# Kernel optimization log

Measured on AMD Instinct MI355X. Metric: run time of the kernel, lower is better.

## Reference

```python
import jax, jax.numpy as jnp
import numpy as np

N_HEAD = 16
D_HEAD = 64
D_MODEL = 1024
SCALE = 1.0 / float(D_HEAD) ** 0.5
LN_EPS = 1e-5


def _rel_shift(x):
    # x: [b, n, i, j] -> Transformer-XL relative shift
    b, n, i, j = x.shape
    x = jnp.pad(x, ((0, 0), (0, 0), (0, 0), (1, 0)))  # zero-pad front of last dim
    x = x.reshape(b, n, j + 1, i)[:, :, 1:, :]
    return x.reshape(b, n, i, j)


def _layer_norm(x, g, b):
    mu = jnp.mean(x, axis=-1, keepdims=True)
    var = jnp.mean(jnp.square(x - mu), axis=-1, keepdims=True)
    return g * (x - mu) / jnp.sqrt(var + LN_EPS) + b


def setup_inputs() -> dict:
    key = jax.random.key(0)
    ks = jax.random.split(key, 8)
    qlen, bsz = 1024, 4
    w = jax.random.normal(ks[0], (qlen, bsz, D_MODEL), jnp.float32)
    r = jax.random.normal(ks[1], (qlen, D_MODEL), jnp.float32)
    r_w_bias = 0.02 * jax.random.normal(ks[2], (N_HEAD, D_HEAD), jnp.float32)
    r_r_bias = 0.02 * jax.random.normal(ks[3], (N_HEAD, D_HEAD), jnp.float32)
    attn_mask = jnp.triu(jnp.ones((qlen, qlen), bool), 1)  # causal, True = masked
    qkv_w = 0.02 * jax.random.normal(ks[4], (D_MODEL, 3 * N_HEAD * D_HEAD), jnp.float32)
    qkv_b = jnp.zeros((3 * N_HEAD * D_HEAD,), jnp.float32)
    rk_w = 0.02 * jax.random.normal(ks[5], (D_MODEL, N_HEAD * D_HEAD), jnp.float32)
    rk_b = jnp.zeros((N_HEAD * D_HEAD,), jnp.float32)
    o_w = 0.02 * jax.random.normal(ks[6], (N_HEAD * D_HEAD, D_MODEL), jnp.float32)
    o_b = jnp.zeros((D_MODEL,), jnp.float32)
    ln_g = jnp.ones((D_MODEL,), jnp.float32)
    ln_b = jnp.zeros((D_MODEL,), jnp.float32)
    return {"w": w, "r": r, "r_w_bias": r_w_bias, "r_r_bias": r_r_bias,
            "qkv_w": qkv_w, "qkv_b": qkv_b, "rk_w": rk_w, "rk_b": rk_b,
            "o_w": o_w, "o_b": o_b, "ln_g": ln_g, "ln_b": ln_b,
            "attn_mask": attn_mask}


def reference(w, r, r_w_bias, r_r_bias, qkv_w, qkv_b, rk_w, rk_b, o_w, o_b, ln_g, ln_b, attn_mask):
    qlen, bsz, _ = w.shape
    # post-lnorm path (pre_lnorm=False)
    heads = w @ qkv_w + qkv_b                       # [q, b, 3*H*D]
    q, k, v = jnp.split(heads, 3, axis=-1)
    q = q.reshape(qlen, bsz, N_HEAD, D_HEAD)
    k = k.reshape(qlen, bsz, N_HEAD, D_HEAD)
    v = v.reshape(qlen, bsz, N_HEAD, D_HEAD)
    rk = (r @ rk_w + rk_b).reshape(-1, N_HEAD, D_HEAD)  # [rlen, H, D]
    AC = jnp.einsum('ibnd,jbnd->bnij', q + r_w_bias, k)
    BD = _rel_shift(jnp.einsum('ibnd,jnd->bnij', q + r_r_bias, rk))
    score = SCALE * (AC + BD)                       # [b, H, q, k]
    score = jnp.where(attn_mask[None, None, :, :], -jnp.inf, score)
    prob = jax.nn.softmax(score, axis=-1)
    vec = jnp.einsum('bnij,jbnd->ibnd', prob, v).reshape(qlen, bsz, N_HEAD * D_HEAD)
    attn_out = vec @ o_w + o_b
    return _layer_norm(w + attn_out, ln_g, ln_b)
```

## Files before the change

### kernel.cpp

```cpp
#include <hip/hip_runtime.h>
#include <math.h>

#define QL 1024
#define BSZ 4
#define NH 16
#define DH 64
#define DM 1024
#define SCALE_F 0.125f

typedef __attribute__((ext_vector_type(8))) short bf16x8;
typedef __attribute__((ext_vector_type(4))) float f32x4;

__device__ __forceinline__ unsigned short f2bf(float f) {
  union { float f; unsigned int u; } c; c.f = f;
  unsigned int u = c.u;
  u += 0x7FFFu + ((u >> 16) & 1u);
  return (unsigned short)(u >> 16);
}
__device__ __forceinline__ float bf2f(unsigned short u) {
  union { unsigned int i; float f; } c; c.i = ((unsigned int)u) << 16;
  return c.f;
}
__device__ __forceinline__ float2 bfp2f(const unsigned short* p) {
  unsigned int u = *(const unsigned int*)p;
  union { unsigned int u; float f; } lo, hi;
  lo.u = (u & 0xFFFFu) << 16;
  hi.u = u & 0xFFFF0000u;
  return make_float2(lo.f, hi.f);
}

__device__ __forceinline__ void ld_lds16(const unsigned short* g, unsigned short* l) {
  __builtin_amdgcn_global_load_lds(
      (const __attribute__((address_space(1))) unsigned int*)g,
      (__attribute__((address_space(3))) unsigned int*)l, 16, 0, 0);
}

__device__ __forceinline__ bf16x8 frag64(const unsigned short* lds, int n, int s) {
  return *(const bf16x8*)(lds + n * 64 + ((s ^ (n & 7)) * 8));
}

template <int CTRL>
__device__ __forceinline__ float dpp_mv(float x) {
  return __int_as_float(__builtin_amdgcn_update_dpp(
      0, __float_as_int(x), CTRL, 0xf, 0xf, true));
}
__device__ __forceinline__ float rowsum16(float x) {
  x += dpp_mv<0x121>(x);
  x += dpp_mv<0x122>(x);
  x += dpp_mv<0x124>(x);
  x += dpp_mv<0x128>(x);
  return x;
}

__global__ __launch_bounds__(256) void prep_kernel(
    const float* __restrict__ w, const float* __restrict__ r,
    const float* __restrict__ qkv_w, const float* __restrict__ rk_w,
    const float* __restrict__ o_w,
    unsigned short* __restrict__ wb, unsigned short* __restrict__ rb,
    unsigned short* __restrict__ qkv_wt, unsigned short* __restrict__ rk_wt,
    unsigned short* __restrict__ o_wt, float* __restrict__ drk) {
  __shared__ __align__(16) unsigned short t[64][72];
  const int bid = blockIdx.x, tid = threadIdx.x;
  if (bid >= 3840) {
    int idx = (bid - 3840) * 256 + tid;
    ((float4*)drk)[idx] = make_float4(0.f, 0.f, 0.f, 0.f);
    return;
  }
  if (bid < 2560) {
    const float* in = (bid < 2048) ? w : r;
    unsigned short* out = (bid < 2048) ? wb : rb;
    int idx = ((bid < 2048) ? bid : (bid - 2048)) * 256 + tid;
    float4 a = *(const float4*)(in + (size_t)idx * 8);
    float4 b = *(const float4*)(in + (size_t)idx * 8 + 4);
    unsigned short o[8] = {f2bf(a.x), f2bf(a.y), f2bf(a.z), f2bf(a.w),
                           f2bf(b.x), f2bf(b.y), f2bf(b.z), f2bf(b.w)};
    *(uint4*)(out + (size_t)idx * 8) = *(const uint4*)o;
    return;
  }
  const float* in; unsigned short* out; int N, n0, k0;
  if (bid < 3328) {
    int l = bid - 2560; in = qkv_w; out = qkv_wt; N = 3072;
    n0 = (l % 48) * 64; k0 = (l / 48) * 64;
  } else if (bid < 3584) {
    int l = bid - 3328; in = rk_w; out = rk_wt; N = 1024;
    n0 = (l & 15) * 64; k0 = (l >> 4) * 64;
  } else {
    int l = bid - 3584; in = o_w; out = o_wt; N = 1024;
    n0 = (l & 15) * 64; k0 = (l >> 4) * 64;
  }
  for (int f = tid; f < 1024; f += 256) {
    int rr = f >> 4, c4 = (f & 15) * 4;
    float4 v = *(const float4*)(in + (size_t)(k0 + rr) * N + n0 + c4);
    t[c4 + 0][rr] = f2bf(v.x); t[c4 + 1][rr] = f2bf(v.y);
    t[c4 + 2][rr] = f2bf(v.z); t[c4 + 3][rr] = f2bf(v.w);
  }
  __syncthreads();
  for (int f = tid; f < 512; f += 256) {
    int rr = f >> 3, seg = (f & 7) * 8;
    *(uint4*)(out + (size_t)(n0 + rr) * 1024 + k0 + seg) = *(const uint4*)&t[rr][seg];
  }
}

__global__ __launch_bounds__(512) void gemm12(
    const unsigned short* __restrict__ wb, const unsigned short* __restrict__ rb,
    const unsigned short* __restrict__ qkv_wt, const unsigned short* __restrict__ rk_wt,
    const float* __restrict__ qkv_b, const float* __restrict__ rk_b,
    const float* __restrict__ rwb, const float* __restrict__ rrb,
    unsigned short* __restrict__ qbf, unsigned short* __restrict__ kbf,
    unsigned short* __restrict__ vtb, unsigned short* __restrict__ rkbf,
    float* __restrict__ drk) {
  __shared__ __align__(16) unsigned short As[2 * 4096];
  __shared__ __align__(16) unsigned short Bs[2 * 4096];
  const int bid = blockIdx.x, tid = threadIdx.x;
  const int w = tid >> 6, lane = tid & 63;
  const int quad = lane >> 4, l15 = lane & 15;
  const int wr = w >> 2, wc = w & 3;
  const bool job0 = bid < 768;
  const unsigned short *A, *BT;
  const float* bias;
  int bm, bn;
  if (job0) {
    A = wb; BT = qkv_wt; bias = qkv_b;
    bn = (bid % 24) * 128; bm = (bid / 24) * 128;
  } else {
    int l = bid - 768;
    A = rb; BT = rk_wt; bias = rk_b;
    bn = (l & 7) * 128; bm = (l >> 3) * 128;
  }
  const int srow = w * 16 + (lane >> 2);
  const int sseg = (lane & 3) ^ ((lane >> 2) & 3);
  f32x4 acc[4][2] = {};

  auto stage = [&](int bf, int k0) {
    ld_lds16(A + (size_t)(bm + srow) * 1024 + k0 + sseg * 8, As + bf * 4096 + w * 512);
    ld_lds16(BT + (size_t)(bn + srow) * 1024 + k0 + sseg * 8, Bs + bf * 4096 + w * 512);
  };

  int buf = 0;
  stage(0, 0);
  for (int k0 = 0; k0 < 1024; k0 += 32) {
    __syncthreads();
    if (k0 + 32 < 1024) stage(buf ^ 1, k0 + 32);
    const unsigned short* Al = As + buf * 4096;
    const unsigned short* Bl = Bs + buf * 4096;
    const int sa = quad ^ (l15 & 3);
    bf16x8 af[4], bfr[2];
#pragma unroll
    for (int rt = 0; rt < 4; ++rt)
      af[rt] = *(const bf16x8*)&Al[(wr * 64 + rt * 16 + l15) * 32 + sa * 8];
#pragma unroll
    for (int nt = 0; nt < 2; ++nt)
      bfr[nt] = *(const bf16x8*)&Bl[(wc * 32 + nt * 16 + l15) * 32 + sa * 8];
#pragma unroll
    for (int rt = 0; rt < 4; ++rt)
#pragma unroll
      for (int nt = 0; nt < 2; ++nt)
        acc[rt][nt] = __builtin_amdgcn_mfma_f32_16x16x32_bf16(af[rt], bfr[nt], acc[rt][nt], 0, 0, 0);
    buf ^= 1;
  }

  if (job0) {
#pragma unroll
    for (int rt = 0; rt < 4; ++rt)
#pragma unroll
      for (int nt = 0; nt < 2; ++nt) {
        int gc = bn + wc * 32 + nt * 16 + l15;
        float bv = bias[gc];
        int part = gc >> 10, h = (gc >> 6) & 15, d = gc & 63;
#pragma unroll
        for (int reg = 0; reg < 4; ++reg) {
          int gr = bm + wr * 64 + rt * 16 + quad * 4 + reg;
          float val = acc[rt][nt][reg] + bv;
          int i = gr >> 2, b = gr & 3;
          if (part == 0)
            qbf[((size_t)((b * NH + h) * QL + i)) * DH + d] = f2bf(val);
          else if (part == 1)
            kbf[((size_t)((b * NH + h) * QL + i)) * DH + d] = f2bf(val);
          else
            vtb[((size_t)((b * NH + h) * DH + d)) * QL + i] = f2bf(val);
        }
      }
  } else {
    const int h = (bn + wc * 32) >> 6;
    float df[2];
#pragma unroll
    for (int nt = 0; nt < 2; ++nt) {
      int dd = (wc & 1) * 32 + nt * 16 + l15;
      df[nt] = rrb[h * DH + dd] - rwb[h * DH + dd];
    }
#pragma unroll
    for (int rt = 0; rt < 4; ++rt) {
      float s[4] = {0.f, 0.f, 0.f, 0.f};
#pragma unroll
      for (int nt = 0; nt < 2; ++nt) {
        int gc = bn + wc * 32 + nt * 16 + l15;
        float bv = bias[gc];
        int d = gc & 63;
#pragma unroll
        for (int reg = 0; reg < 4; ++reg) {
          int gr = bm + wr * 64 + rt * 16 + quad * 4 + reg;
          float val = acc[rt][nt][reg] + bv;
          rkbf[((size_t)(h * QL + gr)) * DH + d] = f2bf(val);
          s[reg] += val * df[nt];
        }
      }
#pragma unroll
      for (int reg = 0; reg < 4; ++reg) {
        float v = s[reg];
        v += __shfl_xor(v, 1);
        v += __shfl_xor(v, 2);
        v += __shfl_xor(v, 4);
        v += __shfl_xor(v, 8);
        if (l15 == 0) {
          int j = bm + wr * 64 + rt * 16 + quad * 4 + reg;
          atomicAdd(&drk[h * QL + j], v);
        }
      }
    }
  }
}

__global__ __launch_bounds__(512) void gemm_o(
    const unsigned short* __restrict__ A, const unsigned short* __restrict__ BT,
    const float* __restrict__ bias, float* __restrict__ Cf) {
  __shared__ __align__(16) unsigned short As[2 * 4096];
  __shared__ __align__(16) unsigned short Bs[2 * 2048];
  const int tid = threadIdx.x;
  const int w = tid >> 6, lane = tid & 63;
  const int quad = lane >> 4, l15 = lane & 15;
  const int wr = w >> 1, wc = w & 1;
  const int bm = blockIdx.y * 128, bn = blockIdx.x * 64;
  const int srow = w * 16 + (lane >> 2);
  const int sseg = (lane & 3) ^ ((lane >> 2) & 3);
  f32x4 acc[2][2] = {};

  auto stage = [&](int bf, int k0) {
    ld_lds16(A + (size_t)(bm + srow) * 1024 + k0 + sseg * 8, As + bf * 4096 + w * 512);
    if (w < 4)
      ld_lds16(BT + (size_t)(bn + srow) * 1024 + k0 + sseg * 8, Bs + bf * 2048 + w * 512);
  };

  int buf = 0;
  stage(0, 0);
  for (int k0 = 0; k0 < 1024; k0 += 32) {
    __syncthreads();
    if (k0 + 32 < 1024) stage(buf ^ 1, k0 + 32);
    const unsigned short* Al = As + buf * 4096;
    const unsigned short* Bl = Bs + buf * 2048;
    const int sa = quad ^ (l15 & 3);
    bf16x8 af[2], bfr[2];
#pragma unroll
    for (int rt = 0; rt < 2; ++rt)
      af[rt] = *(const bf16x8*)&Al[(wr * 32 + rt * 16 + l15) * 32 + sa * 8];
#pragma unroll
    for (int nt = 0; nt < 2; ++nt)
      bfr[nt] = *(const bf16x8*)&Bl[(wc * 32 + nt * 16 + l15) * 32 + sa * 8];
#pragma unroll
    for (int rt = 0; rt < 2; ++rt)
#pragma unroll
      for (int nt = 0; nt < 2; ++nt)
        acc[rt][nt] = __builtin_amdgcn_mfma_f32_16x16x32_bf16(af[rt], bfr[nt], acc[rt][nt], 0, 0, 0);
    buf ^= 1;
  }

#pragma unroll
  for (int rt = 0; rt < 2; ++rt)
#pragma unroll
    for (int nt = 0; nt < 2; ++nt) {
      int gc = bn + wc * 32 + nt * 16 + l15;
      float bv = bias[gc];
#pragma unroll
      for (int reg = 0; reg < 4; ++reg) {
        int gr = bm + wr * 32 + rt * 16 + quad * 4 + reg;
        Cf[(size_t)gr * DM + gc] = acc[rt][nt][reg] + bv;
      }
    }
}

__global__ __launch_bounds__(512, 4) void attn_kernel(
    const unsigned short* __restrict__ qbf, const unsigned short* __restrict__ kbf,
    const unsigned short* __restrict__ vtb, const unsigned short* __restrict__ rkb,
    const float* __restrict__ drk, const float* __restrict__ rwb,
    unsigned short* __restrict__ vecb) {
  __shared__ __align__(16) unsigned short SH[40960];
  unsigned short* Ks = SH;
  unsigned short* Vs = SH + 16384;
  unsigned short* PM = SH + 32768;

  const int tid = threadIdx.x;
  const int w = tid >> 6, lane = tid & 63;
  const int g = w >> 2, wg = w & 3;
  const int quad = lane >> 4, l15 = lane & 15;
  const int bh = blockIdx.x, b = bh >> 4, h = bh & 15;
  const int yA = blockIdx.y;

  const unsigned short* kB0 = kbf + (size_t)bh * QL * DH;
  const unsigned short* vB0 = vtb + (size_t)bh * DH * QL;
  const unsigned short* rB0 = rkb + (size_t)h * QL * DH;
  const float* drkh = drk + h * QL;
  unsigned short* pmw = PM + w * 1024;
  float* ml = (float*)(PM + 4096);

  const int srow8 = lane >> 3, sseg8 = lane & 7;

  for (int stream = 0; stream < 2; ++stream) {
    const int y = (stream == 0) ? (15 - yA) : yA;
    const int i0 = y * 64, tS = y, T = tS + 1;
    const int nR = (T + 1) >> 1;
    const int myBase = g ? nR : 0;
    const int myN = g ? (T - nR) : nR;

    bf16x8 qf[2];
    {
      int qrow = i0 + wg * 16 + l15;
      const unsigned short* qp = qbf + ((size_t)bh * QL + qrow) * DH;
#pragma unroll
      for (int s = 0; s < 2; ++s) {
        int off = s * 32 + quad * 8;
        uint4 raw = *(const uint4*)(qp + off);
        const unsigned short* ru = (const unsigned short*)&raw;
        float4 wb0 = *(const float4*)(rwb + h * DH + off);
        float4 wb1 = *(const float4*)(rwb + h * DH + off + 4);
        union { bf16x8 v; unsigned short u[8]; } qc;
        qc.u[0] = f2bf(bf2f(ru[0]) + wb0.x); qc.u[1] = f2bf(bf2f(ru[1]) + wb0.y);
        qc.u[2] = f2bf(bf2f(ru[2]) + wb0.z); qc.u[3] = f2bf(bf2f(ru[3]) + wb0.w);
        qc.u[4] = f2bf(bf2f(ru[4]) + wb1.x); qc.u[5] = f2bf(bf2f(ru[5]) + wb1.y);
        qc.u[6] = f2bf(bf2f(ru[6]) + wb1.z); qc.u[7] = f2bf(bf2f(ru[7]) + wb1.w);
        qf[s] = qc.v;
      }
    }

    float lrow[4] = {0.f, 0.f, 0.f, 0.f};
    f32x4 pv[4];
#pragma unroll
    for (int r = 0; r < 4; ++r) pv[r] = (f32x4){0.f, 0.f, 0.f, 0.f};

    auto stage_mine = [&](int p, int buf) {
      int tt = min(myBase + p, tS);
      const unsigned short* kb = kB0 + (size_t)(tt * 64) * DH;
      const unsigned short* vb = vB0 + tt * 64;
      unsigned short* kd = Ks + buf * 8192 + g * 4096;
      unsigned short* vd = Vs + buf * 8192 + g * 4096;
#pragma unroll
      for (int ii = 0; ii < 2; ++ii) {
        int row = wg * 16 + ii * 8 + srow8;
        int gs = sseg8 ^ (row & 7);
        ld_lds16(kb + (size_t)row * DH + gs * 8, kd + (wg * 16 + ii * 8) * 64);
        ld_lds16(vb + (size_t)row * QL + gs * 8, vd + (wg * 16 + ii * 8) * 64);
      }
    };

    auto rel_frag = [&](int gb, f32x4& c) {
      int row = min(gb + l15, QL - 1);
      const unsigned short* rp = rB0 + (size_t)row * DH;
      f32x4 a = {0.f, 0.f, 0.f, 0.f};
      a = __builtin_amdgcn_mfma_f32_16x16x32_bf16(qf[0], *(const bf16x8*)(rp + quad * 8), a, 0, 0, 0);
      a = __builtin_amdgcn_mfma_f32_16x16x32_bf16(qf[1], *(const bf16x8*)(rp + 32 + quad * 8), a, 0, 0, 0);
      float dv = drkh[row];
      a[0] += dv; a[1] += dv; a[2] += dv; a[3] += dv;
      c = a;
    };

    f32x4 rc[5];
    {
      const int Bt0 = 1008 - i0 + 64 * myBase - 16 * wg;
#pragma unroll
      for (int f = 0; f < 5; ++f) rel_frag(Bt0 + 16 * f, rc[f]);
    }

    stage_mine(0, 0);
    for (int p = 0; p < nR; ++p) {
      __syncthreads();
      if (p + 1 < nR) stage_mine(p + 1, (p + 1) & 1);
      if (p < myN) {
        const int t = myBase + p;
        const bool diag = (t == tS);
        const unsigned short* ksl = Ks + (p & 1) * 8192 + g * 4096;
        const unsigned short* vsl = Vs + (p & 1) * 8192 + g * 4096;

        if (p > 0) {
          rc[0] = rc[4];
          const int Bt = 1008 - i0 + 64 * t - 16 * wg;
#pragma unroll
          for (int f = 1; f < 5; ++f) rel_frag(Bt + 16 * f, rc[f]);
        }

        f32x4 sacc[4];
#pragma unroll
        for (int nt = 0; nt < 4; ++nt) {
          int n = nt * 16 + l15;
          f32x4 c = {0.f, 0.f, 0.f, 0.f};
          c = __builtin_amdgcn_mfma_f32_16x16x32_bf16(qf[0], frag64(ksl, n, quad), c, 0, 0, 0);
          c = __builtin_amdgcn_mfma_f32_16x16x32_bf16(qf[1], frag64(ksl, n, 4 + quad), c, 0, 0, 0);
          sacc[nt] = c;
        }

#pragma unroll
        for (int r = 0; r < 4; ++r) {
          const int il = wg * 16 + quad * 4 + r;
          const int ls = l15 + 15 - quad * 4 - r;
          const int srcl = (quad << 4) | (ls & 15);
          float rot[5];
#pragma unroll
          for (int f = 0; f < 5; ++f) rot[f] = __shfl(rc[f][r], srcl, 64);
          const bool lo = ls < 16;
          float psum = 0.f;
          const int prow = quad * 4 + r;
          const int psw = prow & 7;
#pragma unroll
          for (int nt = 0; nt < 4; ++nt) {
            float band = lo ? rot[nt] : rot[nt + 1];
            float s = (sacc[nt][r] + band) * SCALE_F;
            if (diag && (nt * 16 + l15) > il) s = -1e30f;
            float e = __expf(s);
            psum += e;
            int jl = nt * 16 + l15;
            pmw[prow * 64 + (((jl >> 3) ^ psw) << 3) + (jl & 7)] = f2bf(e);
          }
          lrow[r] += rowsum16(psum);
        }

        bf16x8 pf0 = frag64(pmw, l15, quad);
        bf16x8 pf1 = frag64(pmw, l15, 4 + quad);
#pragma unroll
        for (int nt = 0; nt < 4; ++nt) {
          int n = nt * 16 + l15;
          pv[nt] = __builtin_amdgcn_mfma_f32_16x16x32_bf16(pf0, frag64(vsl, n, quad), pv[nt], 0, 0, 0);
          pv[nt] = __builtin_amdgcn_mfma_f32_16x16x32_bf16(pf1, frag64(vsl, n, 4 + quad), pv[nt], 0, 0, 0);
        }
      }
    }

    __syncthreads();
    if (g == 1) {
#pragma unroll
      for (int r = 0; r < 4; ++r) {
        int il = wg * 16 + quad * 4 + r;
#pragma unroll
        for (int nt = 0; nt < 4; ++nt)
          PM[il * 64 + nt * 16 + l15] = f2bf(pv[nt][r]);
        if (l15 == 0) ml[il] = lrow[r];
      }
    }
    __syncthreads();
    if (g == 0) {
#pragma unroll
      for (int r = 0; r < 4; ++r) {
        int il = wg * 16 + quad * 4 + r;
        float inv = 1.0f / (lrow[r] + ml[il]);
#pragma unroll
        for (int nt = 0; nt < 4; ++nt) {
          float pv1 = bf2f(PM[il * 64 + nt * 16 + l15]);
          float val = (pv[nt][r] + pv1) * inv;
          vecb[((size_t)((i0 + il) * BSZ + b)) * DM + h * DH + nt * 16 + l15] = f2bf(val);
        }
      }
    }
  }
}

__global__ __launch_bounds__(256) void ln_kernel(
    const float* __restrict__ w, const float* __restrict__ attn,
    const float* __restrict__ g, const float* __restrict__ bta,
    float* __restrict__ out) {
  __shared__ float red[4];
  __shared__ float sval[2];
  const int row = blockIdx.x, tid = threadIdx.x;
  const float* wr = w + (size_t)row * DM;
  const float* ar = attn + (size_t)row * DM;
  float4 wv = *(const float4*)(wr + tid * 4);
  float4 av = *(const float4*)(ar + tid * 4);
  float x0 = wv.x + av.x, x1 = wv.y + av.y, x2 = wv.z + av.z, x3 = wv.w + av.w;
  float s = x0 + x1 + x2 + x3;
#pragma unroll
  for (int off = 32; off; off >>= 1) s += __shfl_down(s, off, 64);
  const int lane = tid & 63, wvi = tid >> 6;
  if (lane == 0) red[wvi] = s;
  __syncthreads();
  if (tid == 0) sval[0] = (red[0] + red[1] + red[2] + red[3]) * (1.0f / 1024.0f);
  __syncthreads();
  const float mu = sval[0];
  float d0 = x0 - mu, d1 = x1 - mu, d2 = x2 - mu, d3 = x3 - mu;
  float vs2 = d0 * d0 + d1 * d1 + d2 * d2 + d3 * d3;
#pragma unroll
  for (int off = 32; off; off >>= 1) vs2 += __shfl_down(vs2, off, 64);
  if (lane == 0) red[wvi] = vs2;
  __syncthreads();
  if (tid == 0)
    sval[1] = rsqrtf((red[0] + red[1] + red[2] + red[3]) * (1.0f / 1024.0f) + 1e-5f);
  __syncthreads();
  const float inv = sval[1];
  float4 gv = *(const float4*)(g + tid * 4);
  float4 bv = *(const float4*)(bta + tid * 4);
  float4 ov;
  ov.x = gv.x * d0 * inv + bv.x;
  ov.y = gv.y * d1 * inv + bv.y;
  ov.z = gv.z * d2 * inv + bv.z;
  ov.w = gv.w * d3 * inv + bv.w;
  *(float4*)(out + (size_t)row * DM + tid * 4) = ov;
}

extern "C" void kernel_launch(void* const* d_in, const int* in_sizes, int n_in,
                              void* d_out, int out_size, void* d_ws, size_t ws_size,
                              hipStream_t stream) {
  const float* w     = (const float*)d_in[0];
  const float* r     = (const float*)d_in[1];
  const float* rwb   = (const float*)d_in[2];
  const float* rrb   = (const float*)d_in[3];
  const float* qkv_w = (const float*)d_in[4];
  const float* qkv_b = (const float*)d_in[5];
  const float* rk_w  = (const float*)d_in[6];
  const float* rk_b  = (const float*)d_in[7];
  const float* o_w   = (const float*)d_in[8];
  const float* o_b   = (const float*)d_in[9];
  const float* ln_g  = (const float*)d_in[10];
  const float* ln_b  = (const float*)d_in[11];

  float* out = (float*)d_out;
  char* p = (char*)d_ws;
  unsigned short* wb     = (unsigned short*)p; p += (size_t)4096 * 1024 * 2;
  unsigned short* rb     = (unsigned short*)p; p += (size_t)1024 * 1024 * 2;
  unsigned short* qkv_wt = (unsigned short*)p; p += (size_t)3072 * 1024 * 2;
  unsigned short* rk_wt  = (unsigned short*)p; p += (size_t)1024 * 1024 * 2;
  unsigned short* o_wt   = (unsigned short*)p; p += (size_t)1024 * 1024 * 2;
  unsigned short* qbf    = (unsigned short*)p; p += (size_t)BSZ * NH * QL * DH * 2;
  unsigned short* kbf    = (unsigned short*)p; p += (size_t)BSZ * NH * QL * DH * 2;
  unsigned short* vtb    = (unsigned short*)p; p += (size_t)BSZ * NH * QL * DH * 2;
  unsigned short* rkbf   = (unsigned short*)p; p += (size_t)NH * QL * DH * 2;
  float*          drk    = (float*)p;          p += (size_t)NH * QL * 4;
  unsigned short* vecb   = (unsigned short*)p; p += (size_t)4096 * 1024 * 2;
  float*          attnf  = (float*)p;          p += (size_t)4096 * 1024 * 4;

  prep_kernel<<<3856, 256, 0, stream>>>(w, r, qkv_w, rk_w, o_w,
                                        wb, rb, qkv_wt, rk_wt, o_wt, drk);
  gemm12<<<832, 512, 0, stream>>>(wb, rb, qkv_wt, rk_wt, qkv_b, rk_b, rwb, rrb,
                                  qbf, kbf, vtb, rkbf, drk);
  attn_kernel<<<dim3(64, 8), 512, 0, stream>>>(qbf, kbf, vtb, rkbf, drk, rwb, vecb);
  gemm_o<<<dim3(16, 32), 512, 0, stream>>>(vecb, o_wt, o_b, attnf);
  ln_kernel<<<4096, 256, 0, stream>>>(w, attnf, ln_g, ln_b, out);
}
```

Before: 290.0 us.

## Halve GEMM block threads with larger per-warp tiles; restructure attention grid and V loads

Both projection GEMMs move from 512 to 256 threads per block, so each warp computes a larger output tile and stages two rows per load. The attention kernel stops pairing a long and a short query block in one workgroup and launches one workgroup per query block (16 in y) with a higher occupancy hint. It also drops V staging in LDS in favour of direct global loads for the PV MFMA, and single-buffers K with an extra barrier. Together these aim for better occupancy and less LDS pressure, at the cost of uncoalesced V reads, less K prefetch overlap and possible load imbalance across blocks.

```diff
diff --git a/kernel.cpp b/kernel.cpp
--- a/kernel.cpp
+++ b/kernel.cpp
@@ -20,13 +20,6 @@
 __device__ __forceinline__ float bf2f(unsigned short u) {
   union { unsigned int i; float f; } c; c.i = ((unsigned int)u) << 16;
   return c.f;
-}
-__device__ __forceinline__ float2 bfp2f(const unsigned short* p) {
-  unsigned int u = *(const unsigned int*)p;
-  union { unsigned int u; float f; } lo, hi;
-  lo.u = (u & 0xFFFFu) << 16;
-  hi.u = u & 0xFFFF0000u;
-  return make_float2(lo.f, hi.f);
 }
 
 __device__ __forceinline__ void ld_lds16(const unsigned short* g, unsigned short* l) {
@@ -101,7 +94,7 @@
   }
 }
 
-__global__ __launch_bounds__(512) void gemm12(
+__global__ __launch_bounds__(256) void gemm12(
     const unsigned short* __restrict__ wb, const unsigned short* __restrict__ rb,
     const unsigned short* __restrict__ qkv_wt, const unsigned short* __restrict__ rk_wt,
     const float* __restrict__ qkv_b, const float* __restrict__ rk_b,
@@ -114,7 +107,7 @@
   const int bid = blockIdx.x, tid = threadIdx.x;
   const int w = tid >> 6, lane = tid & 63;
   const int quad = lane >> 4, l15 = lane & 15;
-  const int wr = w >> 2, wc = w & 3;
+  const int wr = w >> 1, wc = w & 1;
   const bool job0 = bid < 768;
   const unsigned short *A, *BT;
   const float* bias;
@@ -127,13 +120,17 @@
     A = rb; BT = rk_wt; bias = rk_b;
     bn = (l & 7) * 128; bm = (l >> 3) * 128;
   }
-  const int srow = w * 16 + (lane >> 2);
-  const int sseg = (lane & 3) ^ ((lane >> 2) & 3);
-  f32x4 acc[4][2] = {};
+  const int r_ = lane >> 2, sg = lane & 3;
+  const int gs = sg ^ (r_ & 3);
+  f32x4 acc[4][4] = {};
 
   auto stage = [&](int bf, int k0) {
-    ld_lds16(A + (size_t)(bm + srow) * 1024 + k0 + sseg * 8, As + bf * 4096 + w * 512);
-    ld_lds16(BT + (size_t)(bn + srow) * 1024 + k0 + sseg * 8, Bs + bf * 4096 + w * 512);
+#pragma unroll
+    for (int i = 0; i < 2; ++i) {
+      int row = (w * 2 + i) * 16 + r_;
+      ld_lds16(A + (size_t)(bm + row) * 1024 + k0 + gs * 8, As + bf * 4096 + (w * 2 + i) * 512);
+      ld_lds16(BT + (size_t)(bn + row) * 1024 + k0 + gs * 8, Bs + bf * 4096 + (w * 2 + i) * 512);
+    }
   };
 
   int buf = 0;
@@ -144,17 +141,17 @@
     const unsigned short* Al = As + buf * 4096;
     const unsigned short* Bl = Bs + buf * 4096;
     const int sa = quad ^ (l15 & 3);
-    bf16x8 af[4], bfr[2];
+    bf16x8 af[4], bfr[4];
 #pragma unroll
     for (int rt = 0; rt < 4; ++rt)
       af[rt] = *(const bf16x8*)&Al[(wr * 64 + rt * 16 + l15) * 32 + sa * 8];
 #pragma unroll
-    for (int nt = 0; nt < 2; ++nt)
-      bfr[nt] = *(const bf16x8*)&Bl[(wc * 32 + nt * 16 + l15) * 32 + sa * 8];
+    for (int nt = 0; nt < 4; ++nt)
+      bfr[nt] = *(const bf16x8*)&Bl[(wc * 64 + nt * 16 + l15) * 32 + sa * 8];
 #pragma unroll
     for (int rt = 0; rt < 4; ++rt)
 #pragma unroll
-      for (int nt = 0; nt < 2; ++nt)
+      for (int nt = 0; nt < 4; ++nt)
         acc[rt][nt] = __builtin_amdgcn_mfma_f32_16x16x32_bf16(af[rt], bfr[nt], acc[rt][nt], 0, 0, 0);
     buf ^= 1;
   }
@@ -163,8 +160,8 @@
 #pragma unroll
     for (int rt = 0; rt < 4; ++rt)
 #pragma unroll
-      for (int nt = 0; nt < 2; ++nt) {
-        int gc = bn + wc * 32 + nt * 16 + l15;
+      for (int nt = 0; nt < 4; ++nt) {
+        int gc = bn + wc * 64 + nt * 16 + l15;
         float bv = bias[gc];
         int part = gc >> 10, h = (gc >> 6) & 15, d = gc & 63;
 #pragma unroll
@@ -181,19 +178,19 @@
         }
       }
   } else {
-    const int h = (bn + wc * 32) >> 6;
-    float df[2];
-#pragma unroll
-    for (int nt = 0; nt < 2; ++nt) {
-      int dd = (wc & 1) * 32 + nt * 16 + l15;
+    const int h = (bn + wc * 64) >> 6;
+    float df[4];
+#pragma unroll
+    for (int nt = 0; nt < 4; ++nt) {
+      int dd = nt * 16 + l15;
       df[nt] = rrb[h * DH + dd] - rwb[h * DH + dd];
     }
 #pragma unroll
     for (int rt = 0; rt < 4; ++rt) {
       float s[4] = {0.f, 0.f, 0.f, 0.f};
 #pragma unroll
-      for (int nt = 0; nt < 2; ++nt) {
-        int gc = bn + wc * 32 + nt * 16 + l15;
+      for (int nt = 0; nt < 4; ++nt) {
+        int gc = bn + wc * 64 + nt * 16 + l15;
         float bv = bias[gc];
         int d = gc & 63;
 #pragma unroll
@@ -220,7 +217,7 @@
   }
 }
 
-__global__ __launch_bounds__(512) void gemm_o(
+__global__ __launch_bounds__(256) void gemm_o(
     const unsigned short* __restrict__ A, const unsigned short* __restrict__ BT,
     const float* __restrict__ bias, float* __restrict__ Cf) {
   __shared__ __align__(16) unsigned short As[2 * 4096];
@@ -230,14 +227,20 @@
   const int quad = lane >> 4, l15 = lane & 15;
   const int wr = w >> 1, wc = w & 1;
   const int bm = blockIdx.y * 128, bn = blockIdx.x * 64;
-  const int srow = w * 16 + (lane >> 2);
-  const int sseg = (lane & 3) ^ ((lane >> 2) & 3);
-  f32x4 acc[2][2] = {};
+  const int r_ = lane >> 2, sg = lane & 3;
+  const int gs = sg ^ (r_ & 3);
+  f32x4 acc[4][2] = {};
 
   auto stage = [&](int bf, int k0) {
-    ld_lds16(A + (size_t)(bm + srow) * 1024 + k0 + sseg * 8, As + bf * 4096 + w * 512);
-    if (w < 4)
-      ld_lds16(BT + (size_t)(bn + srow) * 1024 + k0 + sseg * 8, Bs + bf * 2048 + w * 512);
+#pragma unroll
+    for (int i = 0; i < 2; ++i) {
+      int row = (w * 2 + i) * 16 + r_;
+      ld_lds16(A + (size_t)(bm + row) * 1024 + k0 + gs * 8, As + bf * 4096 + (w * 2 + i) * 512);
+    }
+    {
+      int row = w * 16 + r_;
+      ld_lds16(BT + (size_t)(bn + row) * 1024 + k0 + gs * 8, Bs + bf * 2048 + w * 512);
+    }
   };
 
   int buf = 0;
@@ -248,15 +251,15 @@
     const unsigned short* Al = As + buf * 4096;
     const unsigned short* Bl = Bs + buf * 2048;
     const int sa = quad ^ (l15 & 3);
-    bf16x8 af[2], bfr[2];
-#pragma unroll
-    for (int rt = 0; rt < 2; ++rt)
-      af[rt] = *(const bf16x8*)&Al[(wr * 32 + rt * 16 + l15) * 32 + sa * 8];
+    bf16x8 af[4], bfr[2];
+#pragma unroll
+    for (int rt = 0; rt < 4; ++rt)
+      af[rt] = *(const bf16x8*)&Al[(wr * 64 + rt * 16 + l15) * 32 + sa * 8];
 #pragma unroll
     for (int nt = 0; nt < 2; ++nt)
       bfr[nt] = *(const bf16x8*)&Bl[(wc * 32 + nt * 16 + l15) * 32 + sa * 8];
 #pragma unroll
-    for (int rt = 0; rt < 2; ++rt)
+    for (int rt = 0; rt < 4; ++rt)
 #pragma unroll
       for (int nt = 0; nt < 2; ++nt)
         acc[rt][nt] = __builtin_amdgcn_mfma_f32_16x16x32_bf16(af[rt], bfr[nt], acc[rt][nt], 0, 0, 0);
@@ -264,35 +267,38 @@
   }
 
 #pragma unroll
-  for (int rt = 0; rt < 2; ++rt)
+  for (int rt = 0; rt < 4; ++rt)
 #pragma unroll
     for (int nt = 0; nt < 2; ++nt) {
       int gc = bn + wc * 32 + nt * 16 + l15;
       float bv = bias[gc];
 #pragma unroll
       for (int reg = 0; reg < 4; ++reg) {
-        int gr = bm + wr * 32 + rt * 16 + quad * 4 + reg;
+        int gr = bm + wr * 64 + rt * 16 + quad * 4 + reg;
         Cf[(size_t)gr * DM + gc] = acc[rt][nt][reg] + bv;
       }
     }
 }
 
-__global__ __launch_bounds__(512, 4) void attn_kernel(
+__global__ __launch_bounds__(512, 6) void attn_kernel(
     const unsigned short* __restrict__ qbf, const unsigned short* __restrict__ kbf,
     const unsigned short* __restrict__ vtb, const unsigned short* __restrict__ rkb,
     const float* __restrict__ drk, const float* __restrict__ rwb,
     unsigned short* __restrict__ vecb) {
-  __shared__ __align__(16) unsigned short SH[40960];
+  __shared__ __align__(16) unsigned short SH[16384];
   unsigned short* Ks = SH;
-  unsigned short* Vs = SH + 16384;
-  unsigned short* PM = SH + 32768;
+  unsigned short* PM = SH + 8192;
 
   const int tid = threadIdx.x;
   const int w = tid >> 6, lane = tid & 63;
   const int g = w >> 2, wg = w & 3;
   const int quad = lane >> 4, l15 = lane & 15;
   const int bh = blockIdx.x, b = bh >> 4, h = bh & 15;
-  const int yA = blockIdx.y;
+  const int y = 15 - (int)blockIdx.y;
+  const int i0 = y * 64, tS = y, T = y + 1;
+  const int nR = (T + 1) >> 1;
+  const int myBase = g ? nR : 0;
+  const int myN = g ? (T - nR) : nR;
 
   const unsigned short* kB0 = kbf + (size_t)bh * QL * DH;
   const unsigned short* vB0 = vtb + (size_t)bh * DH * QL;
@@ -303,157 +309,149 @@
 
   const int srow8 = lane >> 3, sseg8 = lane & 7;
 
-  for (int stream = 0; stream < 2; ++stream) {
-    const int y = (stream == 0) ? (15 - yA) : yA;
-    const int i0 = y * 64, tS = y, T = tS + 1;
-    const int nR = (T + 1) >> 1;
-    const int myBase = g ? nR : 0;
-    const int myN = g ? (T - nR) : nR;
-
-    bf16x8 qf[2];
-    {
-      int qrow = i0 + wg * 16 + l15;
-      const unsigned short* qp = qbf + ((size_t)bh * QL + qrow) * DH;
-#pragma unroll
-      for (int s = 0; s < 2; ++s) {
-        int off = s * 32 + quad * 8;
-        uint4 raw = *(const uint4*)(qp + off);
-        const unsigned short* ru = (const unsigned short*)&raw;
-        float4 wb0 = *(const float4*)(rwb + h * DH + off);
-        float4 wb1 = *(const float4*)(rwb + h * DH + off + 4);
-        union { bf16x8 v; unsigned short u[8]; } qc;
-        qc.u[0] = f2bf(bf2f(ru[0]) + wb0.x); qc.u[1] = f2bf(bf2f(ru[1]) + wb0.y);
-        qc.u[2] = f2bf(bf2f(ru[2]) + wb0.z); qc.u[3] = f2bf(bf2f(ru[3]) + wb0.w);
-        qc.u[4] = f2bf(bf2f(ru[4]) + wb1.x); qc.u[5] = f2bf(bf2f(ru[5]) + wb1.y);
-        qc.u[6] = f2bf(bf2f(ru[6]) + wb1.z); qc.u[7] = f2bf(bf2f(ru[7]) + wb1.w);
-        qf[s] = qc.v;
-      }
-    }
-
-    float lrow[4] = {0.f, 0.f, 0.f, 0.f};
-    f32x4 pv[4];
-#pragma unroll
-    for (int r = 0; r < 4; ++r) pv[r] = (f32x4){0.f, 0.f, 0.f, 0.f};
-
-    auto stage_mine = [&](int p, int buf) {
-      int tt = min(myBase + p, tS);
-      const unsigned short* kb = kB0 + (size_t)(tt * 64) * DH;
-      const unsigned short* vb = vB0 + tt * 64;
-      unsigned short* kd = Ks + buf * 8192 + g * 4096;
-      unsigned short* vd = Vs + buf * 8192 + g * 4096;
-#pragma unroll
-      for (int ii = 0; ii < 2; ++ii) {
-        int row = wg * 16 + ii * 8 + srow8;
-        int gs = sseg8 ^ (row & 7);
-        ld_lds16(kb + (size_t)row * DH + gs * 8, kd + (wg * 16 + ii * 8) * 64);
-        ld_lds16(vb + (size_t)row * QL + gs * 8, vd + (wg * 16 + ii * 8) * 64);
-      }
-    };
-
-    auto rel_frag = [&](int gb, f32x4& c) {
-      int row = min(gb + l15, QL - 1);
-      const unsigned short* rp = rB0 + (size_t)row * DH;
-      f32x4 a = {0.f, 0.f, 0.f, 0.f};
-      a = __builtin_amdgcn_mfma_f32_16x16x32_bf16(qf[0], *(const bf16x8*)(rp + quad * 8), a, 0, 0, 0);
-      a = __builtin_amdgcn_mfma_f32_16x16x32_bf16(qf[1], *(const bf16x8*)(rp + 32 + quad * 8), a, 0, 0, 0);
-      float dv = drkh[row];
-      a[0] += dv; a[1] += dv; a[2] += dv; a[3] += dv;
-      c = a;
-    };
-
-    f32x4 rc[5];
-    {
-      const int Bt0 = 1008 - i0 + 64 * myBase - 16 * wg;
-#pragma unroll
-      for (int f = 0; f < 5; ++f) rel_frag(Bt0 + 16 * f, rc[f]);
-    }
-
-    stage_mine(0, 0);
-    for (int p = 0; p < nR; ++p) {
-      __syncthreads();
-      if (p + 1 < nR) stage_mine(p + 1, (p + 1) & 1);
-      if (p < myN) {
-        const int t = myBase + p;
-        const bool diag = (t == tS);
-        const unsigned short* ksl = Ks + (p & 1) * 8192 + g * 4096;
-        const unsigned short* vsl = Vs + (p & 1) * 8192 + g * 4096;
-
-        if (p > 0) {
-          rc[0] = rc[4];
-          const int Bt = 1008 - i0 + 64 * t - 16 * wg;
-#pragma unroll
-          for (int f = 1; f < 5; ++f) rel_frag(Bt + 16 * f, rc[f]);
+  bf16x8 qf[2];
+  {
+    int qrow = i0 + wg * 16 + l15;
+    const unsigned short* qp = qbf + ((size_t)bh * QL + qrow) * DH;
+#pragma unroll
+    for (int s = 0; s < 2; ++s) {
+      int off = s * 32 + quad * 8;
+      uint4 raw = *(const uint4*)(qp + off);
+      const unsigned short* ru = (const unsigned short*)&raw;
+      float4 wb0 = *(const float4*)(rwb + h * DH + off);
+      float4 wb1 = *(const float4*)(rwb + h * DH + off + 4);
+      union { bf16x8 v; unsigned short u[8]; } qc;
+      qc.u[0] = f2bf(bf2f(ru[0]) + wb0.x); qc.u[1] = f2bf(bf2f(ru[1]) + wb0.y);
+      qc.u[2] = f2bf(bf2f(ru[2]) + wb0.z); qc.u[3] = f2bf(bf2f(ru[3]) + wb0.w);
+      qc.u[4] = f2bf(bf2f(ru[4]) + wb1.x); qc.u[5] = f2bf(bf2f(ru[5]) + wb1.y);
+      qc.u[6] = f2bf(bf2f(ru[6]) + wb1.z); qc.u[7] = f2bf(bf2f(ru[7]) + wb1.w);
+      qf[s] = qc.v;
+    }
+  }
+
+  auto rel_frag = [&](int gb, f32x4& c) {
+    int row = min(gb + l15, QL - 1);
+    const unsigned short* rp = rB0 + (size_t)row * DH;
+    f32x4 a = {0.f, 0.f, 0.f, 0.f};
+    a = __builtin_amdgcn_mfma_f32_16x16x32_bf16(qf[0], *(const bf16x8*)(rp + quad * 8), a, 0, 0, 0);
+    a = __builtin_amdgcn_mfma_f32_16x16x32_bf16(qf[1], *(const bf16x8*)(rp + 32 + quad * 8), a, 0, 0, 0);
+    float dv = drkh[row];
+    a[0] += dv; a[1] += dv; a[2] += dv; a[3] += dv;
+    c = a;
+  };
+
+  auto stage_mine = [&](int p) {
+    int tt = min(myBase + p, tS);
+    const unsigned short* kb = kB0 + (size_t)(tt * 64) * DH;
+    unsigned short* kd = Ks + g * 4096;
+#pragma unroll
+    for (int ii = 0; ii < 2; ++ii) {
+      int row = wg * 16 + ii * 8 + srow8;
+      int gsw = sseg8 ^ (row & 7);
+      ld_lds16(kb + (size_t)row * DH + gsw * 8, kd + (wg * 16 + ii * 8) * 64);
+    }
+  };
+
+  float lrow[4] = {0.f, 0.f, 0.f, 0.f};
+  f32x4 pv[4];
+#pragma unroll
+  for (int r = 0; r < 4; ++r) pv[r] = (f32x4){0.f, 0.f, 0.f, 0.f};
+
+  f32x4 rc[5];
+  {
+    const int Bt0 = 1008 - i0 + 64 * myBase - 16 * wg;
+#pragma unroll
+    for (int f = 0; f < 5; ++f) rel_frag(Bt0 + 16 * f, rc[f]);
+  }
+
+  stage_mine(0);
+  for (int p = 0; p < nR; ++p) {
+    __syncthreads();
+    const int t = myBase + p;
+    const bool active = (p < myN);
+    f32x4 sacc[4];
+    if (active) {
+      const unsigned short* ksl = Ks + g * 4096;
+#pragma unroll
+      for (int nt = 0; nt < 4; ++nt) {
+        int n = nt * 16 + l15;
+        f32x4 c = {0.f, 0.f, 0.f, 0.f};
+        c = __builtin_amdgcn_mfma_f32_16x16x32_bf16(qf[0], frag64(ksl, n, quad), c, 0, 0, 0);
+        c = __builtin_amdgcn_mfma_f32_16x16x32_bf16(qf[1], frag64(ksl, n, 4 + quad), c, 0, 0, 0);
+        sacc[nt] = c;
+      }
+    }
+    __syncthreads();
+    if (p + 1 < nR) stage_mine(p + 1);
+
+    if (active) {
+      const bool diag = (t == tS);
+
+#pragma unroll
+      for (int r = 0; r < 4; ++r) {
+        const int il = wg * 16 + quad * 4 + r;
+        const int ls = l15 + 15 - quad * 4 - r;
+        const int srcl = (quad << 4) | (ls & 15);
+        float rot[5];
+#pragma unroll
+        for (int f = 0; f < 5; ++f) rot[f] = __shfl(rc[f][r], srcl, 64);
+        const bool lo = ls < 16;
+        float psum = 0.f;
+        const int prow = quad * 4 + r;
+        const int psw = prow & 7;
+#pragma unroll
+        for (int nt = 0; nt < 4; ++nt) {
+          float band = lo ? rot[nt] : rot[nt + 1];
+          float s = (sacc[nt][r] + band) * SCALE_F;
+          if (diag && (nt * 16 + l15) > il) s = -1e30f;
+          float e = __expf(s);
+          psum += e;
+          int jl = nt * 16 + l15;
+          pmw[prow * 64 + (((jl >> 3) ^ psw) << 3) + (jl & 7)] = f2bf(e);
         }
-
-        f32x4 sacc[4];
-#pragma unroll
-        for (int nt = 0; nt < 4; ++nt) {
-          int n = nt * 16 + l15;
-          f32x4 c = {0.f, 0.f, 0.f, 0.f};
-          c = __builtin_amdgcn_mfma_f32_16x16x32_bf16(qf[0], frag64(ksl, n, quad), c, 0, 0, 0);
-          c = __builtin_amdgcn_mfma_f32_16x16x32_bf16(qf[1], frag64(ksl, n, 4 + quad), c, 0, 0, 0);
-          sacc[nt] = c;
-        }
-
-#pragma unroll
-        for (int r = 0; r < 4; ++r) {
-          const int il = wg * 16 + quad * 4 + r;
-          const int ls = l15 + 15 - quad * 4 - r;
-          const int srcl = (quad << 4) | (ls & 15);
-          float rot[5];
-#pragma unroll
-          for (int f = 0; f < 5; ++f) rot[f] = __shfl(rc[f][r], srcl, 64);
-          const bool lo = ls < 16;
-          float psum = 0.f;
-          const int prow = quad * 4 + r;
-          const int psw = prow & 7;
-#pragma unroll
-          for (int nt = 0; nt < 4; ++nt) {
-            float band = lo ? rot[nt] : rot[nt + 1];
-            float s = (sacc[nt][r] + band) * SCALE_F;
-            if (diag && (nt * 16 + l15) > il) s = -1e30f;
-            float e = __expf(s);
-            psum += e;
-            int jl = nt * 16 + l15;
-            pmw[prow * 64 + (((jl >> 3) ^ psw) << 3) + (jl & 7)] = f2bf(e);
-          }
-          lrow[r] += rowsum16(psum);
-        }
-
-        bf16x8 pf0 = frag64(pmw, l15, quad);
-        bf16x8 pf1 = frag64(pmw, l15, 4 + quad);
-#pragma unroll
-        for (int nt = 0; nt < 4; ++nt) {
-          int n = nt * 16 + l15;
-          pv[nt] = __builtin_amdgcn_mfma_f32_16x16x32_bf16(pf0, frag64(vsl, n, quad), pv[nt], 0, 0, 0);
-          pv[nt] = __builtin_amdgcn_mfma_f32_16x16x32_bf16(pf1, frag64(vsl, n, 4 + quad), pv[nt], 0, 0, 0);
-        }
-      }
-    }
-
-    __syncthreads();
-    if (g == 1) {
-#pragma unroll
-      for (int r = 0; r < 4; ++r) {
-        int il = wg * 16 + quad * 4 + r;
-#pragma unroll
-        for (int nt = 0; nt < 4; ++nt)
-          PM[il * 64 + nt * 16 + l15] = f2bf(pv[nt][r]);
-        if (l15 == 0) ml[il] = lrow[r];
-      }
-    }
-    __syncthreads();
-    if (g == 0) {
-#pragma unroll
-      for (int r = 0; r < 4; ++r) {
-        int il = wg * 16 + quad * 4 + r;
-        float inv = 1.0f / (lrow[r] + ml[il]);
-#pragma unroll
-        for (int nt = 0; nt < 4; ++nt) {
-          float pv1 = bf2f(PM[il * 64 + nt * 16 + l15]);
-          float val = (pv[nt][r] + pv1) * inv;
-          vecb[((size_t)((i0 + il) * BSZ + b)) * DM + h * DH + nt * 16 + l15] = f2bf(val);
-        }
+        lrow[r] += rowsum16(psum);
+      }
+
+      bf16x8 pf0 = frag64(pmw, l15, quad);
+      bf16x8 pf1 = frag64(pmw, l15, 4 + quad);
+#pragma unroll
+      for (int nt = 0; nt < 4; ++nt) {
+        const unsigned short* vp = vB0 + (size_t)(nt * 16 + l15) * QL + t * 64;
+        pv[nt] = __builtin_amdgcn_mfma_f32_16x16x32_bf16(pf0, *(const bf16x8*)(vp + quad * 8), pv[nt], 0, 0, 0);
+        pv[nt] = __builtin_amdgcn_mfma_f32_16x16x32_bf16(pf1, *(const bf16x8*)(vp + 32 + quad * 8), pv[nt], 0, 0, 0);
+      }
+
+      if (p + 1 < myN) {
+        rc[0] = rc[4];
+        const int Bt = 1008 - i0 + 64 * (t + 1) - 16 * wg;
+#pragma unroll
+        for (int f = 1; f < 5; ++f) rel_frag(Bt + 16 * f, rc[f]);
+      }
+    }
+  }
+
+  __syncthreads();
+  if (g == 1) {
+#pragma unroll
+    for (int r = 0; r < 4; ++r) {
+      int il = wg * 16 + quad * 4 + r;
+#pragma unroll
+      for (int nt = 0; nt < 4; ++nt)
+        PM[il * 64 + nt * 16 + l15] = f2bf(pv[nt][r]);
+      if (l15 == 0) ml[il] = lrow[r];
+    }
+  }
+  __syncthreads();
+  if (g == 0) {
+#pragma unroll
+    for (int r = 0; r < 4; ++r) {
+      int il = wg * 16 + quad * 4 + r;
+      float inv = 1.0f / (lrow[r] + ml[il]);
+#pragma unroll
+      for (int nt = 0; nt < 4; ++nt) {
+        float pv1 = bf2f(PM[il * 64 + nt * 16 + l15]);
+        float val = (pv[nt][r] + pv1) * inv;
+        vecb[((size_t)((i0 + il) * BSZ + b)) * DM + h * DH + nt * 16 + l15] = f2bf(val);
       }
     }
   }
@@ -533,9 +531,9 @@
 
   prep_kernel<<<3856, 256, 0, stream>>>(w, r, qkv_w, rk_w, o_w,
                                         wb, rb, qkv_wt, rk_wt, o_wt, drk);
-  gemm12<<<832, 512, 0, stream>>>(wb, rb, qkv_wt, rk_wt, qkv_b, rk_b, rwb, rrb,
+  gemm12<<<832, 256, 0, stream>>>(wb, rb, qkv_wt, rk_wt, qkv_b, rk_b, rwb, rrb,
                                   qbf, kbf, vtb, rkbf, drk);
-  attn_kernel<<<dim3(64, 8), 512, 0, stream>>>(qbf, kbf, vtb, rkbf, drk, rwb, vecb);
-  gemm_o<<<dim3(16, 32), 512, 0, stream>>>(vecb, o_wt, o_b, attnf);
+  attn_kernel<<<dim3(64, 16), 512, 0, stream>>>(qbf, kbf, vtb, rkbf, drk, rwb, vecb);
+  gemm_o<<<dim3(16, 32), 256, 0, stream>>>(vecb, o_wt, o_b, attnf);
   ln_kernel<<<4096, 256, 0, stream>>>(w, attnf, ln_g, ln_b, out);
 }
```

Result: slower. 414.4 us (+42.9%).
